# Kernel tuning notes

Hardware: AMD Instinct MI355X
Metric: run time of the kernel (lower is better)

The kernel has to match this reference:

```python
import jax, jax.numpy as jnp
import numpy as np

NUM_NODES = 50000
NUM_EDGES = 50000  # hyperedges
NNZ = 500000       # incidence entries
D_IN = 256
D_OUT = 256


def setup_inputs() -> dict:
    key = jax.random.key(0)
    k1, k2, k3, k4, k5, k6 = jax.random.split(key, 6)
    x = jax.random.normal(k1, (NUM_NODES, D_IN), dtype=jnp.float32)
    node_idx = jax.random.randint(k2, (NNZ,), 0, NUM_NODES, dtype=jnp.int64)
    edge_idx = jax.random.randint(k3, (NNZ,), 0, NUM_EDGES, dtype=jnp.int64)
    hyperedge_index = jnp.stack([node_idx, edge_idx], axis=0)
    hyperedge_weight = jax.random.uniform(k4, (NUM_EDGES,), dtype=jnp.float32)
    # PyG Linear(in, heads*out, bias=False) weight, stored here as [in, out]
    W = jax.random.normal(k5, (D_IN, D_OUT), dtype=jnp.float32) / np.sqrt(D_IN)
    b = jax.random.normal(k6, (D_OUT,), dtype=jnp.float32) * 0.01
    return {"x": x, "hyperedge_index": hyperedge_index,
            "hyperedge_weight": hyperedge_weight, "W": W, "b": b}


def reference(x, hyperedge_index, hyperedge_weight, W, b):
    # PyG HypergraphConv, use_attention=False, heads=1, concat=True:
    #   X' = D^{-1} H B^{-1} H^T (X Theta) + bias, with W folded into D.
    num_nodes = x.shape[0]
    num_edges = hyperedge_weight.shape[0]
    node_idx = hyperedge_index[0]
    edge_idx = hyperedge_index[1]

    xl = x @ W  # [N, F] linear transform (no bias in lin)

    # D[i] = sum over incident hyperedges of their weight; invert, inf -> 0
    D = jax.ops.segment_sum(hyperedge_weight[edge_idx], node_idx,
                            num_segments=num_nodes)
    Dinv = jnp.where(D > 0, 1.0 / D, 0.0)

    # B[e] = hyperedge cardinality; invert, inf -> 0
    Bc = jax.ops.segment_sum(jnp.ones((node_idx.shape[0],), dtype=xl.dtype),
                             edge_idx, num_segments=num_edges)
    Binv = jnp.where(Bc > 0, 1.0 / Bc, 0.0)

    # node -> hyperedge: message = B^{-1}[e] * xl[i], summed per hyperedge
    e_feat = jax.ops.segment_sum(Binv[edge_idx][:, None] * xl[node_idx],
                                 edge_idx, num_segments=num_edges)  # [E, F]

    # hyperedge -> node: message = D^{-1}[i] * e_feat[e], summed per node
    out = jax.ops.segment_sum(Dinv[node_idx][:, None] * e_feat[edge_idx],
                              node_idx, num_segments=num_nodes)  # [N, F]

    return out + b
```

## Files before the change

### kernel.cpp

```cpp
#include <hip/hip_runtime.h>
#include <hip/hip_bf16.h>

#define NUM_NODES 50000
#define NUM_EDGES 50000
#define NNZ       500000
#define D_IN      256
#define D_OUT     256
#define HB        128
#define HWORDS    25000
#define CHUNK     3907

typedef __attribute__((ext_vector_type(8))) short  bf16x8;
typedef __attribute__((ext_vector_type(4))) float  f32x4;

static __device__ __forceinline__ float bf2f(unsigned short u) {
    return __uint_as_float(((unsigned)u) << 16);
}
static __device__ __forceinline__ unsigned short f2bf(float f) {
    unsigned u = __float_as_uint(f);
    u += 0x7FFFu + ((u >> 16) & 1u);
    return (unsigned short)(u >> 16);
}

__global__ __launch_bounds__(256) void hist_kernel(
    const int* __restrict__ node_idx, const int* __restrict__ edge_idx,
    unsigned int* __restrict__ HbE, unsigned int* __restrict__ HbN)
{
    const int arr = blockIdx.y;
    const int* __restrict__ idx = arr ? node_idx : edge_idx;
    unsigned int* __restrict__ Hb = arr ? HbN : HbE;
    __shared__ unsigned int h[HWORDS];
    for (int wdi = threadIdx.x; wdi < HWORDS; wdi += 256) h[wdi] = 0;
    __syncthreads();
    int beg = blockIdx.x * CHUNK;
    int end = min(NNZ, beg + CHUNK);
    for (int i = beg + (int)threadIdx.x; i < end; i += 256) {
        int k = idx[i];
        atomicAdd(&h[k >> 1], 1u << ((k & 1) * 16));
    }
    __syncthreads();
    unsigned int* out = Hb + (size_t)blockIdx.x * HWORDS;
    for (int wdi = threadIdx.x; wdi < HWORDS; wdi += 256) out[wdi] = h[wdi];
}

__global__ __launch_bounds__(256) void hreduce_kernel(
    unsigned int* __restrict__ HbE, unsigned int* __restrict__ HbN,
    int* __restrict__ Bc, int* __restrict__ node_cnt)
{
    const int arr = blockIdx.y;
    unsigned int* __restrict__ Hb = arr ? HbN : HbE;
    int* __restrict__ cnt = arr ? node_cnt : Bc;
    int wdi = blockIdx.x * 256 + (int)threadIdx.x;
    if (wdi >= HWORDS) return;
    unsigned int s0 = 0, s1 = 0;
    for (int b = 0; b < HB; ++b) {
        unsigned int u = Hb[(size_t)b * HWORDS + wdi];
        Hb[(size_t)b * HWORDS + wdi] = (s0 & 0xffffu) | (s1 << 16);
        s0 += u & 0xffffu;
        s1 += u >> 16;
    }
    cnt[2 * wdi]     = (int)s0;
    cnt[2 * wdi + 1] = (int)s1;
}

__global__ __launch_bounds__(256) void scan1_kernel(
    const int* __restrict__ cntE, const int* __restrict__ cntN,
    int* __restrict__ offE, int* __restrict__ offN, int* __restrict__ bsums)
{
    const int arr = blockIdx.y;
    const int* cnt = arr ? cntN : cntE;
    int* off       = arr ? offN : offE;
    int tid = threadIdx.x;
    int i = blockIdx.x * 256 + tid;
    int v = (i < 50000) ? cnt[i] : 0;
    __shared__ int sh[256];
    sh[tid] = v;
    __syncthreads();
    for (int s = 1; s < 256; s <<= 1) {
        int t = (tid >= s) ? sh[tid - s] : 0;
        __syncthreads();
        sh[tid] += t;
        __syncthreads();
    }
    if (i < 50000) off[i] = sh[tid] - v;
    if (tid == 255) bsums[arr * 196 + blockIdx.x] = sh[255];
}

__global__ __launch_bounds__(256) void scan2_kernel(
    const int* __restrict__ bsums, int* __restrict__ bsum_off)
{
    __shared__ int sh[256];
    int tid = threadIdx.x;
    for (int arr = 0; arr < 2; ++arr) {
        int v = (tid < 196) ? bsums[arr * 196 + tid] : 0;
        sh[tid] = v;
        __syncthreads();
        for (int s = 1; s < 256; s <<= 1) {
            int t = (tid >= s) ? sh[tid - s] : 0;
            __syncthreads();
            sh[tid] += t;
            __syncthreads();
        }
        if (tid < 196) bsum_off[arr * 196 + tid] = sh[tid] - v;
        __syncthreads();
    }
}

__global__ __launch_bounds__(256) void scan3_kernel(
    const int* __restrict__ bsum_off, int* __restrict__ offE, int* __restrict__ offN)
{
    const int arr = blockIdx.y;
    int* off = arr ? offN : offE;
    int i = blockIdx.x * 256 + threadIdx.x;
    if (i < 50000) off[i] += bsum_off[arr * 196 + blockIdx.x];
    if (blockIdx.x == 0 && threadIdx.x == 0) off[50000] = NNZ;
}

__global__ __launch_bounds__(256) void fill_kernel(
    const int* __restrict__ node_idx, const int* __restrict__ edge_idx,
    const unsigned int* __restrict__ HbE, const unsigned int* __restrict__ HbN,
    const int* __restrict__ edge_off, const int* __restrict__ node_off,
    int* __restrict__ edge_nodes, int* __restrict__ node_edges)
{
    const int arr = blockIdx.y;
    const int* __restrict__ key = arr ? node_idx : edge_idx;
    const int* __restrict__ val = arr ? edge_idx : node_idx;
    const unsigned int* __restrict__ Hb = arr ? HbN : HbE;
    const int* __restrict__ off = arr ? node_off : edge_off;
    int* __restrict__ out       = arr ? node_edges : edge_nodes;

    __shared__ unsigned int h[HWORDS];
    const unsigned int* hrow = Hb + (size_t)blockIdx.x * HWORDS;
    for (int wdi = threadIdx.x; wdi < HWORDS; wdi += 256) h[wdi] = hrow[wdi];
    __syncthreads();

    int beg = blockIdx.x * CHUNK;
    int end = min(NNZ, beg + CHUNK);
    for (int i = beg + (int)threadIdx.x; i < end; i += 256) {
        int k = key[i];
        int sh = (k & 1) * 16;
        unsigned int old = atomicAdd(&h[k >> 1], 1u << sh);
        int rank = (int)((old >> sh) & 0xffffu);
        out[off[k] + rank] = val[i];
    }
}

__global__ __launch_bounds__(256) void transpose_w_kernel(
    const float* __restrict__ W, unsigned short* __restrict__ Wt)
{
    int n = blockIdx.x, k = threadIdx.x;
    Wt[n * 256 + k] = f2bf(W[k * 256 + n]);
}

__global__ __launch_bounds__(256) void gemm_kernel(
    const float* __restrict__ x, const unsigned short* __restrict__ Wt,
    unsigned short* __restrict__ xl)
{
    __shared__ __align__(16) unsigned short sA[64 * 32];
    __shared__ __align__(16) unsigned short sB[256 * 32];

    const int tid  = threadIdx.x;
    const int l    = tid & 63;
    const int wq   = tid >> 6;
    const int quad = l >> 4;
    const int l15  = l & 15;
    const int m0   = blockIdx.x * 64;

    f32x4 acc[4][4];
    #pragma unroll
    for (int i = 0; i < 4; ++i)
        #pragma unroll
        for (int j = 0; j < 4; ++j) acc[i][j] = (f32x4){0.f, 0.f, 0.f, 0.f};

    const int ar = tid >> 2, ag = tid & 3;
    int agm = m0 + ar; if (agm > NUM_NODES - 1) agm = NUM_NODES - 1;
    const float* aptr = x + (size_t)agm * D_IN + ag * 8;
    unsigned short* aout = &sA[ar * 32 + (ag ^ ((ar >> 1) & 3)) * 8];

    for (int k0 = 0; k0 < D_IN; k0 += 32) {
        {
            float4 v0 = *(const float4*)(aptr + k0);
            float4 v1 = *(const float4*)(aptr + k0 + 4);
            bf16x8 av;
            av[0] = (short)f2bf(v0.x); av[1] = (short)f2bf(v0.y);
            av[2] = (short)f2bf(v0.z); av[3] = (short)f2bf(v0.w);
            av[4] = (short)f2bf(v1.x); av[5] = (short)f2bf(v1.y);
            av[6] = (short)f2bf(v1.z); av[7] = (short)f2bf(v1.w);
            *(bf16x8*)aout = av;
        }
        #pragma unroll
        for (int i = 0; i < 4; ++i) {
            int c = i * 256 + tid;
            int row = c >> 2, g = c & 3;
            bf16x8 bv = *(const bf16x8*)(Wt + row * 256 + k0 + g * 8);
            int s = g ^ ((row >> 1) & 3);
            *(bf16x8*)(&sB[row * 32 + s * 8]) = bv;
        }
        __syncthreads();

        bf16x8 af[4], bfr[4];
        #pragma unroll
        for (int mi = 0; mi < 4; ++mi) {
            int r = mi * 16 + l15;
            int s = quad ^ ((r >> 1) & 3);
            af[mi] = *(const bf16x8*)(&sA[r * 32 + s * 8]);
        }
        #pragma unroll
        for (int ni = 0; ni < 4; ++ni) {
            int r = wq * 64 + ni * 16 + l15;
            int s = quad ^ ((r >> 1) & 3);
            bfr[ni] = *(const bf16x8*)(&sB[r * 32 + s * 8]);
        }
        #pragma unroll
        for (int mi = 0; mi < 4; ++mi)
            #pragma unroll
            for (int ni = 0; ni < 4; ++ni)
                acc[mi][ni] = __builtin_amdgcn_mfma_f32_16x16x32_bf16(
                    af[mi], bfr[ni], acc[mi][ni], 0, 0, 0);
        __syncthreads();
    }

    #pragma unroll
    for (int mi = 0; mi < 4; ++mi) {
        #pragma unroll
        for (int ni = 0; ni < 4; ++ni) {
            int col = wq * 64 + ni * 16 + l15;
            #pragma unroll
            for (int r = 0; r < 4; ++r) {
                int m = m0 + mi * 16 + quad * 4 + r;
                if (m < NUM_NODES)
                    xl[(size_t)m * D_OUT + col] = f2bf(acc[mi][ni][r]);
            }
        }
    }
}

__global__ __launch_bounds__(256) void edge_agg_kernel(
    const unsigned short* __restrict__ xl,
    const int* __restrict__ edge_off, const int* __restrict__ edge_nodes,
    unsigned short* __restrict__ e_feat)
{
    int e = blockIdx.x * 4 + (threadIdx.x >> 6);
    int lane = threadIdx.x & 63;
    if (e >= NUM_EDGES) return;
    int beg = edge_off[e], end = edge_off[e + 1];
    float ax = 0.f, ay = 0.f, az = 0.f, aw = 0.f;
    int j = beg;
    for (; j + 4 <= end; j += 4) {
        int n0 = edge_nodes[j];
        int n1 = edge_nodes[j + 1];
        int n2 = edge_nodes[j + 2];
        int n3 = edge_nodes[j + 3];
        ushort4 u0 = *(const ushort4*)(xl + (size_t)n0 * D_OUT + lane * 4);
        ushort4 u1 = *(const ushort4*)(xl + (size_t)n1 * D_OUT + lane * 4);
        ushort4 u2 = *(const ushort4*)(xl + (size_t)n2 * D_OUT + lane * 4);
        ushort4 u3 = *(const ushort4*)(xl + (size_t)n3 * D_OUT + lane * 4);
        ax += bf2f(u0.x) + bf2f(u1.x) + bf2f(u2.x) + bf2f(u3.x);
        ay += bf2f(u0.y) + bf2f(u1.y) + bf2f(u2.y) + bf2f(u3.y);
        az += bf2f(u0.z) + bf2f(u1.z) + bf2f(u2.z) + bf2f(u3.z);
        aw += bf2f(u0.w) + bf2f(u1.w) + bf2f(u2.w) + bf2f(u3.w);
    }
    for (; j < end; ++j) {
        int node = edge_nodes[j];
        ushort4 u = *(const ushort4*)(xl + (size_t)node * D_OUT + lane * 4);
        ax += bf2f(u.x); ay += bf2f(u.y); az += bf2f(u.z); aw += bf2f(u.w);
    }
    float binv = (end > beg) ? 1.0f / (float)(end - beg) : 0.0f;
    ushort4 o;
    o.x = f2bf(ax * binv); o.y = f2bf(ay * binv);
    o.z = f2bf(az * binv); o.w = f2bf(aw * binv);
    *(ushort4*)(e_feat + (size_t)e * D_OUT + lane * 4) = o;
}

__global__ __launch_bounds__(256) void node_agg_kernel(
    const unsigned short* __restrict__ e_feat,
    const int* __restrict__ node_off, const int* __restrict__ node_edges,
    const float* __restrict__ w, const float* __restrict__ bias,
    float* __restrict__ out)
{
    int n = blockIdx.x * 4 + (threadIdx.x >> 6);
    int lane = threadIdx.x & 63;
    if (n >= NUM_NODES) return;
    int beg = node_off[n], end = node_off[n + 1];
    float ax = 0.f, ay = 0.f, az = 0.f, aw = 0.f;
    float dsum = 0.f;
    int j = beg;
    for (; j + 4 <= end; j += 4) {
        int e0 = node_edges[j];
        int e1 = node_edges[j + 1];
        int e2 = node_edges[j + 2];
        int e3 = node_edges[j + 3];
        ushort4 u0 = *(const ushort4*)(e_feat + (size_t)e0 * D_OUT + lane * 4);
        ushort4 u1 = *(const ushort4*)(e_feat + (size_t)e1 * D_OUT + lane * 4);
        ushort4 u2 = *(const ushort4*)(e_feat + (size_t)e2 * D_OUT + lane * 4);
        ushort4 u3 = *(const ushort4*)(e_feat + (size_t)e3 * D_OUT + lane * 4);
        dsum += w[e0] + w[e1] + w[e2] + w[e3];
        ax += bf2f(u0.x) + bf2f(u1.x) + bf2f(u2.x) + bf2f(u3.x);
        ay += bf2f(u0.y) + bf2f(u1.y) + bf2f(u2.y) + bf2f(u3.y);
        az += bf2f(u0.z) + bf2f(u1.z) + bf2f(u2.z) + bf2f(u3.z);
        aw += bf2f(u0.w) + bf2f(u1.w) + bf2f(u2.w) + bf2f(u3.w);
    }
    for (; j < end; ++j) {
        int e = node_edges[j];
        dsum += w[e];
        ushort4 u = *(const ushort4*)(e_feat + (size_t)e * D_OUT + lane * 4);
        ax += bf2f(u.x); ay += bf2f(u.y); az += bf2f(u.z); aw += bf2f(u.w);
    }
    float dinv = (dsum > 0.0f) ? 1.0f / dsum : 0.0f;
    float4 bv = *(const float4*)(bias + lane * 4);
    float4 o;
    o.x = ax * dinv + bv.x;
    o.y = ay * dinv + bv.y;
    o.z = az * dinv + bv.z;
    o.w = aw * dinv + bv.w;
    *(float4*)(out + (size_t)n * D_OUT + lane * 4) = o;
}

extern "C" void kernel_launch(void* const* d_in, const int* in_sizes, int n_in,
                              void* d_out, int out_size, void* d_ws, size_t ws_size,
                              hipStream_t stream) {
    const float* x    = (const float*)d_in[0];
    const int*   hidx = (const int*)d_in[1];
    const float* w    = (const float*)d_in[2];
    const float* W    = (const float*)d_in[3];
    const float* b    = (const float*)d_in[4];
    const int* node_idx = hidx;
    const int* edge_idx = hidx + NNZ;

    char* ws = (char*)d_ws;
    size_t off = 0;
    auto alloc = [&](size_t bytes) -> void* {
        off = (off + 511) & ~(size_t)511;
        void* p = ws + off;
        off += bytes;
        return p;
    };
    unsigned short* xl     = (unsigned short*)alloc((size_t)NUM_NODES * D_OUT * 2);
    unsigned short* e_feat = (unsigned short*)alloc((size_t)NUM_EDGES * D_OUT * 2);
    int* Bc         = (int*)alloc(50000 * sizeof(int));
    int* node_cnt   = (int*)alloc(50000 * sizeof(int));
    int* edge_off   = (int*)alloc((NUM_EDGES + 1) * sizeof(int));
    int* node_off   = (int*)alloc((NUM_NODES + 1) * sizeof(int));
    int* edge_nodes = (int*)alloc((size_t)NNZ * sizeof(int));
    int* node_edges = (int*)alloc((size_t)NNZ * sizeof(int));
    unsigned short* Wt = (unsigned short*)alloc(256 * 256 * 2);
    int* bsums    = (int*)alloc(392 * sizeof(int));
    int* bsum_off = (int*)alloc(392 * sizeof(int));

    unsigned int* HbE = (unsigned int*)xl;
    unsigned int* HbN = (unsigned int*)e_feat;

    hist_kernel<<<dim3(HB, 2), 256, 0, stream>>>(node_idx, edge_idx, HbE, HbN);
    hreduce_kernel<<<dim3((HWORDS + 255) / 256, 2), 256, 0, stream>>>(HbE, HbN, Bc, node_cnt);
    scan1_kernel<<<dim3(196, 2), 256, 0, stream>>>(Bc, node_cnt, edge_off, node_off, bsums);
    scan2_kernel<<<1, 256, 0, stream>>>(bsums, bsum_off);
    scan3_kernel<<<dim3(196, 2), 256, 0, stream>>>(bsum_off, edge_off, node_off);
    fill_kernel<<<dim3(HB, 2), 256, 0, stream>>>(node_idx, edge_idx, HbE, HbN,
                                                 edge_off, node_off, edge_nodes, node_edges);
    transpose_w_kernel<<<256, 256, 0, stream>>>(W, Wt);
    gemm_kernel<<<(NUM_NODES + 63) / 64, 256, 0, stream>>>(x, Wt, xl);
    edge_agg_kernel<<<NUM_EDGES / 4, 256, 0, stream>>>(xl, edge_off, edge_nodes, e_feat);
    node_agg_kernel<<<NUM_NODES / 4, 256, 0, stream>>>(e_feat, node_off, node_edges, w, b,
                                                       (float*)d_out);
}
```

Measured before the change: 254.7 us.

## Drop scan3 and transpose kernels, restructure GEMM, deepen gather unrolling

Folds the W transpose into the histogram kernel and removes the scan3 pass: consumers now add the per-block scan offset (bsum_off) on the fly, and scan2 writes the end sentinel. The GEMM now keeps a 32-row A tile fully in shared memory, double-buffers the W tiles with register prefetch, and stores through a shared-memory bounce buffer for vectorized bf16 writes. Both aggregation kernels unroll gathers to 8 independent loads to raise memory-level parallelism. The aim is fewer launches and better latency hiding, at the cost of extra index math and more shared memory in the GEMM.

```diff
diff --git a/kernel.cpp b/kernel.cpp
--- a/kernel.cpp
+++ b/kernel.cpp
@@ -9,6 +9,7 @@
 #define HB        128
 #define HWORDS    25000
 #define CHUNK     3907
+#define NBLK      196
 
 typedef __attribute__((ext_vector_type(8))) short  bf16x8;
 typedef __attribute__((ext_vector_type(4))) float  f32x4;
@@ -24,9 +25,14 @@
 
 __global__ __launch_bounds__(256) void hist_kernel(
     const int* __restrict__ node_idx, const int* __restrict__ edge_idx,
-    unsigned int* __restrict__ HbE, unsigned int* __restrict__ HbN)
+    unsigned int* __restrict__ HbE, unsigned int* __restrict__ HbN,
+    const float* __restrict__ W, unsigned short* __restrict__ Wt)
 {
     const int arr = blockIdx.y;
+    {
+        int n = arr * HB + blockIdx.x;
+        Wt[n * 256 + threadIdx.x] = f2bf(W[(size_t)threadIdx.x * 256 + n]);
+    }
     const int* __restrict__ idx = arr ? node_idx : edge_idx;
     unsigned int* __restrict__ Hb = arr ? HbN : HbE;
     __shared__ unsigned int h[HWORDS];
@@ -83,16 +89,17 @@
         __syncthreads();
     }
     if (i < 50000) off[i] = sh[tid] - v;
-    if (tid == 255) bsums[arr * 196 + blockIdx.x] = sh[255];
+    if (tid == 255) bsums[arr * NBLK + blockIdx.x] = sh[255];
 }
 
 __global__ __launch_bounds__(256) void scan2_kernel(
-    const int* __restrict__ bsums, int* __restrict__ bsum_off)
+    const int* __restrict__ bsums, int* __restrict__ bsum_off,
+    int* __restrict__ offE, int* __restrict__ offN)
 {
     __shared__ int sh[256];
     int tid = threadIdx.x;
     for (int arr = 0; arr < 2; ++arr) {
-        int v = (tid < 196) ? bsums[arr * 196 + tid] : 0;
+        int v = (tid < NBLK) ? bsums[arr * NBLK + tid] : 0;
         sh[tid] = v;
         __syncthreads();
         for (int s = 1; s < 256; s <<= 1) {
@@ -101,25 +108,20 @@
             sh[tid] += t;
             __syncthreads();
         }
-        if (tid < 196) bsum_off[arr * 196 + tid] = sh[tid] - v;
-        __syncthreads();
-    }
-}
-
-__global__ __launch_bounds__(256) void scan3_kernel(
-    const int* __restrict__ bsum_off, int* __restrict__ offE, int* __restrict__ offN)
-{
-    const int arr = blockIdx.y;
-    int* off = arr ? offN : offE;
-    int i = blockIdx.x * 256 + threadIdx.x;
-    if (i < 50000) off[i] += bsum_off[arr * 196 + blockIdx.x];
-    if (blockIdx.x == 0 && threadIdx.x == 0) off[50000] = NNZ;
+        if (tid < NBLK) bsum_off[arr * NBLK + tid] = sh[tid] - v;
+        if (tid == NBLK - 1) {
+            int* off = arr ? offN : offE;
+            off[50000] = NNZ - (sh[tid] - v);
+        }
+        __syncthreads();
+    }
 }
 
 __global__ __launch_bounds__(256) void fill_kernel(
     const int* __restrict__ node_idx, const int* __restrict__ edge_idx,
     const unsigned int* __restrict__ HbE, const unsigned int* __restrict__ HbN,
     const int* __restrict__ edge_off, const int* __restrict__ node_off,
+    const int* __restrict__ bsum_off,
     int* __restrict__ edge_nodes, int* __restrict__ node_edges)
 {
     const int arr = blockIdx.y;
@@ -127,6 +129,7 @@
     const int* __restrict__ val = arr ? edge_idx : node_idx;
     const unsigned int* __restrict__ Hb = arr ? HbN : HbE;
     const int* __restrict__ off = arr ? node_off : edge_off;
+    const int* __restrict__ bs  = bsum_off + arr * NBLK;
     int* __restrict__ out       = arr ? node_edges : edge_nodes;
 
     __shared__ unsigned int h[HWORDS];
@@ -141,124 +144,149 @@
         int sh = (k & 1) * 16;
         unsigned int old = atomicAdd(&h[k >> 1], 1u << sh);
         int rank = (int)((old >> sh) & 0xffffu);
-        out[off[k] + rank] = val[i];
-    }
-}
-
-__global__ __launch_bounds__(256) void transpose_w_kernel(
-    const float* __restrict__ W, unsigned short* __restrict__ Wt)
-{
-    int n = blockIdx.x, k = threadIdx.x;
-    Wt[n * 256 + k] = f2bf(W[k * 256 + n]);
+        out[off[k] + bs[k >> 8] + rank] = val[i];
+    }
 }
 
 __global__ __launch_bounds__(256) void gemm_kernel(
     const float* __restrict__ x, const unsigned short* __restrict__ Wt,
     unsigned short* __restrict__ xl)
 {
-    __shared__ __align__(16) unsigned short sA[64 * 32];
-    __shared__ __align__(16) unsigned short sB[256 * 32];
+    __shared__ __align__(16) unsigned short sA[32 * 256];
+    __shared__ __align__(16) unsigned short sB[2][256 * 32];
 
     const int tid  = threadIdx.x;
     const int l    = tid & 63;
     const int wq   = tid >> 6;
     const int quad = l >> 4;
     const int l15  = l & 15;
-    const int m0   = blockIdx.x * 64;
-
-    f32x4 acc[4][4];
-    #pragma unroll
-    for (int i = 0; i < 4; ++i)
-        #pragma unroll
-        for (int j = 0; j < 4; ++j) acc[i][j] = (f32x4){0.f, 0.f, 0.f, 0.f};
-
-    const int ar = tid >> 2, ag = tid & 3;
-    int agm = m0 + ar; if (agm > NUM_NODES - 1) agm = NUM_NODES - 1;
-    const float* aptr = x + (size_t)agm * D_IN + ag * 8;
-    unsigned short* aout = &sA[ar * 32 + (ag ^ ((ar >> 1) & 3)) * 8];
-
-    for (int k0 = 0; k0 < D_IN; k0 += 32) {
-        {
-            float4 v0 = *(const float4*)(aptr + k0);
-            float4 v1 = *(const float4*)(aptr + k0 + 4);
+    const int m0   = blockIdx.x * 32;
+
+    {
+        int row = tid >> 3;
+        int kb  = (tid & 7) * 32;
+        int gm = m0 + row; if (gm > NUM_NODES - 1) gm = NUM_NODES - 1;
+        const float* p = x + (size_t)gm * D_IN + kb;
+        #pragma unroll
+        for (int j = 0; j < 4; ++j) {
+            float4 v0 = *(const float4*)(p + j * 8);
+            float4 v1 = *(const float4*)(p + j * 8 + 4);
             bf16x8 av;
             av[0] = (short)f2bf(v0.x); av[1] = (short)f2bf(v0.y);
             av[2] = (short)f2bf(v0.z); av[3] = (short)f2bf(v0.w);
             av[4] = (short)f2bf(v1.x); av[5] = (short)f2bf(v1.y);
             av[6] = (short)f2bf(v1.z); av[7] = (short)f2bf(v1.w);
-            *(bf16x8*)aout = av;
-        }
+            int u  = (kb >> 3) + j;
+            int us = u ^ (row & 7);
+            *(bf16x8*)(&sA[row * 256 + us * 8]) = av;
+        }
+    }
+    bf16x8 breg[4];
+    #pragma unroll
+    for (int i = 0; i < 4; ++i) {
+        int c = i * 256 + tid, row = c >> 2, g = c & 3;
+        breg[i] = *(const bf16x8*)(Wt + row * 256 + g * 8);
+    }
+
+    f32x4 acc[2][4];
+    #pragma unroll
+    for (int i = 0; i < 2; ++i)
+        #pragma unroll
+        for (int j = 0; j < 4; ++j) acc[i][j] = (f32x4){0.f, 0.f, 0.f, 0.f};
+
+    int buf = 0;
+    for (int k0 = 0; k0 < 8; ++k0) {
         #pragma unroll
         for (int i = 0; i < 4; ++i) {
-            int c = i * 256 + tid;
-            int row = c >> 2, g = c & 3;
-            bf16x8 bv = *(const bf16x8*)(Wt + row * 256 + k0 + g * 8);
+            int c = i * 256 + tid, row = c >> 2, g = c & 3;
             int s = g ^ ((row >> 1) & 3);
-            *(bf16x8*)(&sB[row * 32 + s * 8]) = bv;
-        }
-        __syncthreads();
-
-        bf16x8 af[4], bfr[4];
-        #pragma unroll
-        for (int mi = 0; mi < 4; ++mi) {
-            int r = mi * 16 + l15;
-            int s = quad ^ ((r >> 1) & 3);
-            af[mi] = *(const bf16x8*)(&sA[r * 32 + s * 8]);
-        }
+            *(bf16x8*)(&sB[buf][row * 32 + s * 8]) = breg[i];
+        }
+        __syncthreads();
+        if (k0 < 7) {
+            #pragma unroll
+            for (int i = 0; i < 4; ++i) {
+                int c = i * 256 + tid, row = c >> 2, g = c & 3;
+                breg[i] = *(const bf16x8*)(Wt + row * 256 + (k0 + 1) * 32 + g * 8);
+            }
+        }
+        bf16x8 af[2];
+        #pragma unroll
+        for (int mi = 0; mi < 2; ++mi) {
+            int r  = mi * 16 + l15;
+            int u  = k0 * 4 + quad;
+            int us = u ^ (r & 7);
+            af[mi] = *(const bf16x8*)(&sA[r * 256 + us * 8]);
+        }
+        bf16x8 bfr[4];
         #pragma unroll
         for (int ni = 0; ni < 4; ++ni) {
             int r = wq * 64 + ni * 16 + l15;
             int s = quad ^ ((r >> 1) & 3);
-            bfr[ni] = *(const bf16x8*)(&sB[r * 32 + s * 8]);
-        }
-        #pragma unroll
-        for (int mi = 0; mi < 4; ++mi)
+            bfr[ni] = *(const bf16x8*)(&sB[buf][r * 32 + s * 8]);
+        }
+        #pragma unroll
+        for (int mi = 0; mi < 2; ++mi)
             #pragma unroll
             for (int ni = 0; ni < 4; ++ni)
                 acc[mi][ni] = __builtin_amdgcn_mfma_f32_16x16x32_bf16(
                     af[mi], bfr[ni], acc[mi][ni], 0, 0, 0);
-        __syncthreads();
-    }
-
-    #pragma unroll
-    for (int mi = 0; mi < 4; ++mi) {
+        buf ^= 1;
+    }
+
+    float* bounce = (float*)&sB[0][0];
+    for (int half = 0; half < 2; ++half) {
+        __syncthreads();
         #pragma unroll
         for (int ni = 0; ni < 4; ++ni) {
             int col = wq * 64 + ni * 16 + l15;
             #pragma unroll
-            for (int r = 0; r < 4; ++r) {
-                int m = m0 + mi * 16 + quad * 4 + r;
-                if (m < NUM_NODES)
-                    xl[(size_t)m * D_OUT + col] = f2bf(acc[mi][ni][r]);
-            }
+            for (int r = 0; r < 4; ++r)
+                bounce[(quad * 4 + r) * 260 + col] = acc[half][ni][r];
+        }
+        __syncthreads();
+        int row = tid >> 4;
+        int c0  = (tid & 15) * 16;
+        int gm  = m0 + half * 16 + row;
+        if (gm < NUM_NODES) {
+            const float* src = bounce + row * 260 + c0;
+            bf16x8 o0, o1;
+            #pragma unroll
+            for (int j = 0; j < 8; ++j) o0[j] = (short)f2bf(src[j]);
+            #pragma unroll
+            for (int j = 0; j < 8; ++j) o1[j] = (short)f2bf(src[8 + j]);
+            *(bf16x8*)(xl + (size_t)gm * D_OUT + c0)     = o0;
+            *(bf16x8*)(xl + (size_t)gm * D_OUT + c0 + 8) = o1;
         }
     }
 }
 
 __global__ __launch_bounds__(256) void edge_agg_kernel(
     const unsigned short* __restrict__ xl,
-    const int* __restrict__ edge_off, const int* __restrict__ edge_nodes,
+    const int* __restrict__ edge_off, const int* __restrict__ bsE,
+    const int* __restrict__ edge_nodes,
     unsigned short* __restrict__ e_feat)
 {
     int e = blockIdx.x * 4 + (threadIdx.x >> 6);
     int lane = threadIdx.x & 63;
     if (e >= NUM_EDGES) return;
-    int beg = edge_off[e], end = edge_off[e + 1];
+    int beg = edge_off[e]     + bsE[e >> 8];
+    int end = edge_off[e + 1] + bsE[(e + 1) >> 8];
     float ax = 0.f, ay = 0.f, az = 0.f, aw = 0.f;
     int j = beg;
-    for (; j + 4 <= end; j += 4) {
-        int n0 = edge_nodes[j];
-        int n1 = edge_nodes[j + 1];
-        int n2 = edge_nodes[j + 2];
-        int n3 = edge_nodes[j + 3];
-        ushort4 u0 = *(const ushort4*)(xl + (size_t)n0 * D_OUT + lane * 4);
-        ushort4 u1 = *(const ushort4*)(xl + (size_t)n1 * D_OUT + lane * 4);
-        ushort4 u2 = *(const ushort4*)(xl + (size_t)n2 * D_OUT + lane * 4);
-        ushort4 u3 = *(const ushort4*)(xl + (size_t)n3 * D_OUT + lane * 4);
-        ax += bf2f(u0.x) + bf2f(u1.x) + bf2f(u2.x) + bf2f(u3.x);
-        ay += bf2f(u0.y) + bf2f(u1.y) + bf2f(u2.y) + bf2f(u3.y);
-        az += bf2f(u0.z) + bf2f(u1.z) + bf2f(u2.z) + bf2f(u3.z);
-        aw += bf2f(u0.w) + bf2f(u1.w) + bf2f(u2.w) + bf2f(u3.w);
+    for (; j + 8 <= end; j += 8) {
+        int nn[8];
+        #pragma unroll
+        for (int t = 0; t < 8; ++t) nn[t] = edge_nodes[j + t];
+        ushort4 uu[8];
+        #pragma unroll
+        for (int t = 0; t < 8; ++t)
+            uu[t] = *(const ushort4*)(xl + (size_t)nn[t] * D_OUT + lane * 4);
+        #pragma unroll
+        for (int t = 0; t < 8; ++t) {
+            ax += bf2f(uu[t].x); ay += bf2f(uu[t].y);
+            az += bf2f(uu[t].z); aw += bf2f(uu[t].w);
+        }
     }
     for (; j < end; ++j) {
         int node = edge_nodes[j];
@@ -274,31 +302,36 @@
 
 __global__ __launch_bounds__(256) void node_agg_kernel(
     const unsigned short* __restrict__ e_feat,
-    const int* __restrict__ node_off, const int* __restrict__ node_edges,
+    const int* __restrict__ node_off, const int* __restrict__ bsN,
+    const int* __restrict__ node_edges,
     const float* __restrict__ w, const float* __restrict__ bias,
     float* __restrict__ out)
 {
     int n = blockIdx.x * 4 + (threadIdx.x >> 6);
     int lane = threadIdx.x & 63;
     if (n >= NUM_NODES) return;
-    int beg = node_off[n], end = node_off[n + 1];
+    int beg = node_off[n]     + bsN[n >> 8];
+    int end = node_off[n + 1] + bsN[(n + 1) >> 8];
     float ax = 0.f, ay = 0.f, az = 0.f, aw = 0.f;
     float dsum = 0.f;
     int j = beg;
-    for (; j + 4 <= end; j += 4) {
-        int e0 = node_edges[j];
-        int e1 = node_edges[j + 1];
-        int e2 = node_edges[j + 2];
-        int e3 = node_edges[j + 3];
-        ushort4 u0 = *(const ushort4*)(e_feat + (size_t)e0 * D_OUT + lane * 4);
-        ushort4 u1 = *(const ushort4*)(e_feat + (size_t)e1 * D_OUT + lane * 4);
-        ushort4 u2 = *(const ushort4*)(e_feat + (size_t)e2 * D_OUT + lane * 4);
-        ushort4 u3 = *(const ushort4*)(e_feat + (size_t)e3 * D_OUT + lane * 4);
-        dsum += w[e0] + w[e1] + w[e2] + w[e3];
-        ax += bf2f(u0.x) + bf2f(u1.x) + bf2f(u2.x) + bf2f(u3.x);
-        ay += bf2f(u0.y) + bf2f(u1.y) + bf2f(u2.y) + bf2f(u3.y);
-        az += bf2f(u0.z) + bf2f(u1.z) + bf2f(u2.z) + bf2f(u3.z);
-        aw += bf2f(u0.w) + bf2f(u1.w) + bf2f(u2.w) + bf2f(u3.w);
+    for (; j + 8 <= end; j += 8) {
+        int ee[8];
+        #pragma unroll
+        for (int t = 0; t < 8; ++t) ee[t] = node_edges[j + t];
+        ushort4 uu[8];
+        #pragma unroll
+        for (int t = 0; t < 8; ++t)
+            uu[t] = *(const ushort4*)(e_feat + (size_t)ee[t] * D_OUT + lane * 4);
+        float ws[8];
+        #pragma unroll
+        for (int t = 0; t < 8; ++t) ws[t] = w[ee[t]];
+        #pragma unroll
+        for (int t = 0; t < 8; ++t) {
+            dsum += ws[t];
+            ax += bf2f(uu[t].x); ay += bf2f(uu[t].y);
+            az += bf2f(uu[t].z); aw += bf2f(uu[t].w);
+        }
     }
     for (; j < end; ++j) {
         int e = node_edges[j];
@@ -344,22 +377,22 @@
     int* edge_nodes = (int*)alloc((size_t)NNZ * sizeof(int));
     int* node_edges = (int*)alloc((size_t)NNZ * sizeof(int));
     unsigned short* Wt = (unsigned short*)alloc(256 * 256 * 2);
-    int* bsums    = (int*)alloc(392 * sizeof(int));
-    int* bsum_off = (int*)alloc(392 * sizeof(int));
+    int* bsums    = (int*)alloc(2 * NBLK * sizeof(int));
+    int* bsum_off = (int*)alloc(2 * NBLK * sizeof(int));
 
     unsigned int* HbE = (unsigned int*)xl;
     unsigned int* HbN = (unsigned int*)e_feat;
 
-    hist_kernel<<<dim3(HB, 2), 256, 0, stream>>>(node_idx, edge_idx, HbE, HbN);
+    hist_kernel<<<dim3(HB, 2), 256, 0, stream>>>(node_idx, edge_idx, HbE, HbN, W, Wt);
     hreduce_kernel<<<dim3((HWORDS + 255) / 256, 2), 256, 0, stream>>>(HbE, HbN, Bc, node_cnt);
-    scan1_kernel<<<dim3(196, 2), 256, 0, stream>>>(Bc, node_cnt, edge_off, node_off, bsums);
-    scan2_kernel<<<1, 256, 0, stream>>>(bsums, bsum_off);
-    scan3_kernel<<<dim3(196, 2), 256, 0, stream>>>(bsum_off, edge_off, node_off);
+    scan1_kernel<<<dim3(NBLK, 2), 256, 0, stream>>>(Bc, node_cnt, edge_off, node_off, bsums);
+    scan2_kernel<<<1, 256, 0, stream>>>(bsums, bsum_off, edge_off, node_off);
     fill_kernel<<<dim3(HB, 2), 256, 0, stream>>>(node_idx, edge_idx, HbE, HbN,
-                                                 edge_off, node_off, edge_nodes, node_edges);
-    transpose_w_kernel<<<256, 256, 0, stream>>>(W, Wt);
-    gemm_kernel<<<(NUM_NODES + 63) / 64, 256, 0, stream>>>(x, Wt, xl);
-    edge_agg_kernel<<<NUM_EDGES / 4, 256, 0, stream>>>(xl, edge_off, edge_nodes, e_feat);
-    node_agg_kernel<<<NUM_NODES / 4, 256, 0, stream>>>(e_feat, node_off, node_edges, w, b,
-                                                       (float*)d_out);
-}
+                                                 edge_off, node_off, bsum_off,
+                                                 edge_nodes, node_edges);
+    gemm_kernel<<<(NUM_NODES + 31) / 32, 256, 0, stream>>>(x, Wt, xl);
+    edge_agg_kernel<<<NUM_EDGES / 4, 256, 0, stream>>>(xl, edge_off, bsum_off,
+                                                       edge_nodes, e_feat);
+    node_agg_kernel<<<NUM_NODES / 4, 256, 0, stream>>>(e_feat, node_off, bsum_off + NBLK,
+                                                       node_edges, w, b, (float*)d_out);
+}
```

Result: no change. 253.7 us (-0.4%).
